# Kernel optimization log

Hardware: AMD Instinct MI355X
Metric: run time of the kernel (lower is better)

The kernel has to match this reference:

```python
import jax, jax.numpy as jnp
import numpy as np

C = 256
C8 = C // 8


def setup_inputs() -> dict:
    key = jax.random.key(0)
    ks = jax.random.split(key, 9)
    B, H, W = 4, 64, 64
    s = 1.0 / np.sqrt(C)
    return {
        "pre_feat": jax.random.normal(ks[0], (B, C, H, W), jnp.float32),
        "post_feat": jax.random.normal(ks[1], (B, C, H, W), jnp.float32),
        "Wq": jax.random.normal(ks[2], (C8, C), jnp.float32) * s,
        "bq": jnp.zeros((C8,), jnp.float32),
        "Wk": jax.random.normal(ks[3], (C8, C), jnp.float32) * s,
        "bk": jnp.zeros((C8,), jnp.float32),
        "Wv": jax.random.normal(ks[4], (C, C), jnp.float32) * s,
        "bv": jnp.zeros((C,), jnp.float32),
        "gamma": jnp.zeros((1,), jnp.float32),
    }


def reference(pre_feat, post_feat, Wq, bq, Wk, bk, Wv, bv, gamma):
    B, Cc, H, W = pre_feat.shape
    N = H * W
    pre = pre_feat.reshape(B, Cc, N)    # (B, C, N)
    post = post_feat.reshape(B, Cc, N)
    # 1x1 convs == per-pixel linear projections
    q = jnp.einsum('dc,bcn->bdn', Wq, post) + bq[None, :, None]  # (B, C8, N)
    k = jnp.einsum('dc,bcn->bdn', Wk, pre) + bk[None, :, None]   # (B, C8, N)
    v = jnp.einsum('dc,bcn->bdn', Wv, pre) + bv[None, :, None]   # (B, C, N)
    # energy[b,i,j] = <q[b,:,i], k[b,:,j]>  (unscaled)
    energy = jnp.einsum('bdi,bdj->bij', q, k)                    # (B, N, N)
    attention = jax.nn.softmax(energy, axis=-1)
    # out[b,c,i] = sum_j v[b,c,j] * attention[b,i,j]
    out = jnp.einsum('bcj,bij->bci', v, attention).reshape(B, Cc, H, W)
    return gamma[0] * out + post_feat
```

## Files before the change

kernel.cpp:

```cpp
#include <hip/hip_runtime.h>
#include <hip/hip_bf16.h>

#define Bn 4
#define Cn 256
#define Dn 32
#define Nn 4096

typedef __bf16 bf16x8 __attribute__((ext_vector_type(8)));
typedef float f32x4 __attribute__((ext_vector_type(4)));

__device__ __forceinline__ float bf2f(unsigned short u) {
  unsigned int v = ((unsigned int)u) << 16;
  return __builtin_bit_cast(float, v);
}
__device__ __forceinline__ unsigned short f2bf(float f) {
  unsigned int v = __builtin_bit_cast(unsigned int, f);
  v += 0x7FFFu + ((v >> 16) & 1u);
  return (unsigned short)(v >> 16);
}
__device__ __forceinline__ unsigned int pk2(float a, float b) {
  union { __hip_bfloat162 h; unsigned int u; } x;
  x.h = __float22bfloat162_rn(make_float2(a, b));
  return x.u;
}
__device__ __forceinline__ bf16x8 ldfrag(const unsigned short* p) {
  return __builtin_bit_cast(bf16x8, *(const uint4*)p);
}
__device__ __forceinline__ uint4 pack8(const float* p) {
  float4 a = *(const float4*)p;
  float4 b = *(const float4*)(p + 4);
  union { unsigned int u2[4]; uint4 u; } x;
  x.u2[0] = pk2(a.x, a.y); x.u2[1] = pk2(a.z, a.w);
  x.u2[2] = pk2(b.x, b.y); x.u2[3] = pk2(b.z, b.w);
  return x.u;
}
__device__ __forceinline__ bf16x8 ldfrag_f32(const float* p) {
  float4 a = *(const float4*)p;
  float4 b = *(const float4*)(p + 4);
  union { unsigned int u2[4]; bf16x8 v; } x;
  x.u2[0] = pk2(a.x, a.y); x.u2[1] = pk2(a.z, a.w);
  x.u2[2] = pk2(b.x, b.y); x.u2[3] = pk2(b.z, b.w);
  return x.v;
}
__device__ __forceinline__ void async16(unsigned short* lds, const unsigned short* g) {
  __builtin_amdgcn_global_load_lds(
      (const __attribute__((address_space(1))) unsigned int*)g,
      (__attribute__((address_space(3))) unsigned int*)lds, 16, 0, 0);
}

__global__ __launch_bounds__(256) void qkprep(
    const float* __restrict__ pre, const float* __restrict__ post,
    const float* __restrict__ Wq, const float* __restrict__ bq,
    const float* __restrict__ Wk, const float* __restrict__ bk,
    const float* __restrict__ Wv,
    unsigned short* __restrict__ Qt, unsigned short* __restrict__ Kt,
    unsigned short* __restrict__ preBf, unsigned short* __restrict__ WvBf)
{
  const int blk = blockIdx.x, tid = threadIdx.x;
  if (blk >= 512) {
    if (blk < 1024) {
      size_t base = ((size_t)(blk - 512) * 256 + tid) * 32;
#pragma unroll
      for (int u = 0; u < 4; u++)
        *(uint4*)(preBf + base + u * 8) = pack8(pre + base + u * 8);
    } else {
      size_t base = ((size_t)(blk - 1024) * 256 + tid) * 32;
#pragma unroll
      for (int u = 0; u < 4; u++)
        *(uint4*)(WvBf + base + u * 8) = pack8(Wv + base + u * 8);
    }
    return;
  }
  const int lane = tid & 63, w = tid >> 6;
  const int quad = lane >> 4, n16 = lane & 15;
  const int b = blk >> 7;
  const int i0 = (blk & 127) << 5;
  const int isub = w & 1, dh = w >> 1;
  const int i = i0 + isub * 16 + n16;

  const f32x4 zz = {0.f, 0.f, 0.f, 0.f};
  f32x4 aq = zz, ak = zz;
  const float* postB = post + (size_t)b * Cn * Nn + i;
  const float* preB  = pre  + (size_t)b * Cn * Nn + i;

#pragma unroll
  for (int kc = 0; kc < 8; kc++) {
    const int c0 = kc * 32 + quad * 8;
    const float* pp = postB + (size_t)c0 * Nn;
    const float* pr = preB + (size_t)c0 * Nn;
    union { unsigned int u2[4]; bf16x8 v; } bp, bq8;
#pragma unroll
    for (int e2 = 0; e2 < 4; e2++) {
      float p0 = pp[(size_t)(2 * e2) * Nn], p1 = pp[(size_t)(2 * e2 + 1) * Nn];
      float r0 = pr[(size_t)(2 * e2) * Nn], r1 = pr[(size_t)(2 * e2 + 1) * Nn];
      bp.u2[e2] = pk2(p0, p1);
      bq8.u2[e2] = pk2(r0, r1);
    }
    bf16x8 awq = ldfrag_f32(Wq + (size_t)(dh * 16 + n16) * Cn + kc * 32 + quad * 8);
    bf16x8 awk = ldfrag_f32(Wk + (size_t)(dh * 16 + n16) * Cn + kc * 32 + quad * 8);
    aq = __builtin_amdgcn_mfma_f32_16x16x32_bf16(awq, bp.v, aq, 0, 0, 0);
    ak = __builtin_amdgcn_mfma_f32_16x16x32_bf16(awk, bq8.v, ak, 0, 0, 0);
  }
  const float LOG2E = 1.44269504f;
  union { unsigned short s[4]; uint2 u; } oq, ok;
#pragma unroll
  for (int r = 0; r < 4; r++) {
    int d = dh * 16 + quad * 4 + r;
    oq.s[r] = f2bf((aq[r] + bq[d]) * LOG2E);
    ok.s[r] = f2bf(ak[r] + bk[d]);
  }
  *(uint2*)(Qt + ((size_t)b * Nn + i) * Dn + dh * 16 + quad * 4) = oq.u;
  *(uint2*)(Kt + ((size_t)b * Nn + i) * Dn + dh * 16 + quad * 4) = ok.u;
}

__global__ __launch_bounds__(256, 4) void flash_attn(
    const unsigned short* __restrict__ Qt, const unsigned short* __restrict__ Kt,
    const unsigned short* __restrict__ preBf,
    unsigned short* __restrict__ Opart, float* __restrict__ Lpart)
{
  __shared__ __align__(16) unsigned short sX[256 * 64];
  __shared__ __align__(16) unsigned short Pl[64 * 64];

  const int tid = threadIdx.x;
  const int lane = tid & 63, w = tid >> 6;
  const int quad = lane >> 4, n16 = lane & 15;
  const int b = blockIdx.x >> 8;
  const int js = (blockIdx.x >> 6) & 3;
  const int it = blockIdx.x & 63;
  const int i0 = it * 64;
  const int jbase = js * 1024;

  const bf16x8 qf = ldfrag(Qt + ((size_t)b * Nn + i0 + w * 16 + n16) * Dn + quad * 8);

  const f32x4 zz = {0.f, 0.f, 0.f, 0.f};
  f32x4 acc[4][4];
#pragma unroll
  for (int sub = 0; sub < 4; sub++)
#pragma unroll
    for (int ct = 0; ct < 4; ct++) acc[sub][ct] = zz;
  float lrow = 0.f;

  const size_t laneoff = (size_t)(lane >> 3) * Nn + (size_t)(((lane & 7) ^ (lane >> 3)) << 3);
  const unsigned short* preB = preBf + (size_t)b * Cn * Nn + laneoff;
  const int xsw = n16 & 7;
  const int xoff0 = (quad ^ xsw) << 3;
  const int xoff1 = ((4 + quad) ^ xsw) << 3;
  const int psw = (n16 & 7) << 3;

  for (int t = 0; t < 16; ++t) {
    const int j0 = jbase + t * 64;
    __syncthreads();
#pragma unroll
    for (int k = 0; k < 8; k++) {
      const int rb = (k * 4 + w) * 8;
      async16(sX + rb * 64 + (lane << 3), preB + (size_t)rb * Nn + j0);
    }
    {
      f32x4 sc[4];
#pragma unroll
      for (int jt = 0; jt < 4; jt++) {
        bf16x8 akf = ldfrag(Kt + ((size_t)b * Nn + j0 + jt * 16 + n16) * Dn + quad * 8);
        sc[jt] = __builtin_amdgcn_mfma_f32_16x16x32_bf16(akf, qf, zz, 0, 0, 0);
      }
      float ps = 0.f;
#pragma unroll
      for (int jt = 0; jt < 4; jt++) {
        float p0 = exp2f(fminf(sc[jt][0], 101.f));
        float p1 = exp2f(fminf(sc[jt][1], 101.f));
        float p2 = exp2f(fminf(sc[jt][2], 101.f));
        float p3 = exp2f(fminf(sc[jt][3], 101.f));
        ps += (p0 + p1) + (p2 + p3);
        union { unsigned int u2[2]; uint2 u; } pk;
        pk.u2[0] = pk2(p0, p1);
        pk.u2[1] = pk2(p2, p3);
        *(uint2*)&Pl[(size_t)(w * 16 + n16) * 64 + ((jt * 16 + quad * 4) ^ psw)] = pk.u;
      }
      ps += __shfl_xor(ps, 16);
      ps += __shfl_xor(ps, 32);
      lrow += ps;
    }
    __syncthreads();

#pragma unroll
    for (int kc = 0; kc < 2; kc++) {
      const int xo = kc ? xoff1 : xoff0;
      bf16x8 pB[4];
#pragma unroll
      for (int sub = 0; sub < 4; sub++)
        pB[sub] = ldfrag(&Pl[(size_t)(sub * 16 + n16) * 64 + ((kc * 32 + quad * 8) ^ psw)]);
#pragma unroll
      for (int ct = 0; ct < 4; ct++) {
        const int crow = w * 64 + ct * 16 + n16;
        bf16x8 av = ldfrag(&sX[crow * 64 + xo]);
        acc[0][ct] = __builtin_amdgcn_mfma_f32_16x16x32_bf16(av, pB[0], acc[0][ct], 0, 0, 0);
        acc[1][ct] = __builtin_amdgcn_mfma_f32_16x16x32_bf16(av, pB[1], acc[1][ct], 0, 0, 0);
        acc[2][ct] = __builtin_amdgcn_mfma_f32_16x16x32_bf16(av, pB[2], acc[2][ct], 0, 0, 0);
        acc[3][ct] = __builtin_amdgcn_mfma_f32_16x16x32_bf16(av, pB[3], acc[3][ct], 0, 0, 0);
      }
    }
  }

  const size_t pbase = (size_t)(js * 4 + b) * Nn;
  if (quad == 0) Lpart[pbase + i0 + w * 16 + n16] = lrow;
#pragma unroll
  for (int sub = 0; sub < 4; sub++) {
    const int i = i0 + sub * 16 + n16;
#pragma unroll
    for (int ct = 0; ct < 4; ct++) {
      union { unsigned int u2[2]; uint2 u; } pk;
      pk.u2[0] = pk2(acc[sub][ct][0], acc[sub][ct][1]);
      pk.u2[1] = pk2(acc[sub][ct][2], acc[sub][ct][3]);
      *(uint2*)(Opart + (pbase + i) * 256 + w * 64 + ct * 16 + quad * 4) = pk.u;
    }
  }
}

__global__ __launch_bounds__(256) void combine(
    const unsigned short* __restrict__ Opart, const float* __restrict__ Lpart,
    const unsigned short* __restrict__ WvBf, const float* __restrict__ bv,
    const float* __restrict__ post, const float* __restrict__ gamma,
    float* __restrict__ out)
{
  __shared__ __align__(16) unsigned short sU[16 * 264];
  __shared__ float sL[16];

  const int tid = threadIdx.x;
  const int lane = tid & 63, w = tid >> 6;
  const int quad = lane >> 4, n16 = lane & 15;
  const int b = blockIdx.x >> 8;
  const int i0 = (blockIdx.x & 255) << 4;

  if (tid < 16) {
    float l = 0.f;
#pragma unroll
    for (int js = 0; js < 4; js++) l += Lpart[(size_t)(js * 4 + b) * Nn + i0 + tid];
    sL[tid] = 1.f / l;
  }
  __syncthreads();

#pragma unroll
  for (int pass = 0; pass < 2; pass++) {
    const int s = tid + pass * 256;
    const int il = s >> 5, c8 = (s & 31) << 3;
    const float inv = sL[il];
    float a[8] = {0.f, 0.f, 0.f, 0.f, 0.f, 0.f, 0.f, 0.f};
#pragma unroll
    for (int js = 0; js < 4; js++) {
      uint4 uu = *(const uint4*)(Opart + ((size_t)(js * 4 + b) * Nn + i0 + il) * 256 + c8);
      const unsigned short* us = (const unsigned short*)&uu;
#pragma unroll
      for (int e = 0; e < 8; e++) a[e] += bf2f(us[e]);
    }
    union { unsigned int u2[4]; uint4 u; } pk;
#pragma unroll
    for (int e2 = 0; e2 < 4; e2++) pk.u2[e2] = pk2(a[2 * e2] * inv, a[2 * e2 + 1] * inv);
    *(uint4*)&sU[il * 264 + c8] = pk.u;
  }
  __syncthreads();

  bf16x8 ub[8];
#pragma unroll
  for (int kc = 0; kc < 8; kc++)
    ub[kc] = ldfrag(&sU[n16 * 264 + kc * 32 + quad * 8]);

  const float g = gamma[0];
  const f32x4 zz = {0.f, 0.f, 0.f, 0.f};
#pragma unroll
  for (int e = 0; e < 4; e++) {
    const int ct2 = w * 4 + e;
    f32x4 o = zz;
#pragma unroll
    for (int kc = 0; kc < 8; kc++) {
      bf16x8 awv = ldfrag(WvBf + (size_t)(ct2 * 16 + n16) * Cn + kc * 32 + quad * 8);
      o = __builtin_amdgcn_mfma_f32_16x16x32_bf16(awv, ub[kc], o, 0, 0, 0);
    }
#pragma unroll
    for (int r = 0; r < 4; r++) {
      const int c = ct2 * 16 + quad * 4 + r;
      const size_t addr = ((size_t)b * Cn + c) * Nn + i0 + n16;
      out[addr] = g * (o[r] + bv[c]) + post[addr];
    }
  }
}

extern "C" void kernel_launch(void* const* d_in, const int* in_sizes, int n_in,
                              void* d_out, int out_size, void* d_ws, size_t ws_size,
                              hipStream_t stream) {
  const float* pre   = (const float*)d_in[0];
  const float* post  = (const float*)d_in[1];
  const float* Wq    = (const float*)d_in[2];
  const float* bq    = (const float*)d_in[3];
  const float* Wk    = (const float*)d_in[4];
  const float* bk    = (const float*)d_in[5];
  const float* Wv    = (const float*)d_in[6];
  const float* bv    = (const float*)d_in[7];
  const float* gamma = (const float*)d_in[8];
  float* out = (float*)d_out;

  unsigned short* ws = (unsigned short*)d_ws;
  unsigned short* Qt    = ws;
  unsigned short* Kt    = Qt + (size_t)Bn * Nn * Dn;
  unsigned short* preBf = Kt + (size_t)Bn * Nn * Dn;
  unsigned short* WvBf  = preBf + (size_t)Bn * Cn * Nn;
  float* Lpart = (float*)(WvBf + Cn * Cn);
  unsigned short* Opart = (unsigned short*)(Lpart + 4 * Bn * Nn);

  qkprep<<<1032, 256, 0, stream>>>(pre, post, Wq, bq, Wk, bk, Wv,
                                   Qt, Kt, preBf, WvBf);
  flash_attn<<<1024, 256, 0, stream>>>(Qt, Kt, preBf, Opart, Lpart);
  combine<<<1024, 256, 0, stream>>>(Opart, Lpart, WvBf, bv, post, gamma, out);
}
```

Baseline: 188.2 us.

## Compute V projection before attention and simplify combine to transpose-add

```diff
diff --git a/kernel.cpp b/kernel.cpp
--- a/kernel.cpp
+++ b/kernel.cpp
@@ -25,14 +25,6 @@
 }
 __device__ __forceinline__ bf16x8 ldfrag(const unsigned short* p) {
   return __builtin_bit_cast(bf16x8, *(const uint4*)p);
-}
-__device__ __forceinline__ uint4 pack8(const float* p) {
-  float4 a = *(const float4*)p;
-  float4 b = *(const float4*)(p + 4);
-  union { unsigned int u2[4]; uint4 u; } x;
-  x.u2[0] = pk2(a.x, a.y); x.u2[1] = pk2(a.z, a.w);
-  x.u2[2] = pk2(b.x, b.y); x.u2[3] = pk2(b.z, b.w);
-  return x.u;
 }
 __device__ __forceinline__ bf16x8 ldfrag_f32(const float* p) {
   float4 a = *(const float4*)p;
@@ -52,33 +44,58 @@
     const float* __restrict__ pre, const float* __restrict__ post,
     const float* __restrict__ Wq, const float* __restrict__ bq,
     const float* __restrict__ Wk, const float* __restrict__ bk,
-    const float* __restrict__ Wv,
+    const float* __restrict__ Wv, const float* __restrict__ bv,
     unsigned short* __restrict__ Qt, unsigned short* __restrict__ Kt,
-    unsigned short* __restrict__ preBf, unsigned short* __restrict__ WvBf)
+    unsigned short* __restrict__ VBf)
 {
   const int blk = blockIdx.x, tid = threadIdx.x;
-  if (blk >= 512) {
-    if (blk < 1024) {
-      size_t base = ((size_t)(blk - 512) * 256 + tid) * 32;
-#pragma unroll
-      for (int u = 0; u < 4; u++)
-        *(uint4*)(preBf + base + u * 8) = pack8(pre + base + u * 8);
-    } else {
-      size_t base = ((size_t)(blk - 1024) * 256 + tid) * 32;
-#pragma unroll
-      for (int u = 0; u < 4; u++)
-        *(uint4*)(WvBf + base + u * 8) = pack8(Wv + base + u * 8);
-    }
-    return;
-  }
   const int lane = tid & 63, w = tid >> 6;
   const int quad = lane >> 4, n16 = lane & 15;
+  const f32x4 zz = {0.f, 0.f, 0.f, 0.f};
+
+  if (blk >= 512) {
+    const int vb = blk - 512;
+    const int b = vb >> 7;
+    const int j0 = (vb & 127) << 5;
+    const int jsub = w & 1, chalf = w >> 1;
+    const int j = j0 + jsub * 16 + n16;
+
+    f32x4 acc[8];
+#pragma unroll
+    for (int ct = 0; ct < 8; ct++) acc[ct] = zz;
+
+    const float* preB = pre + (size_t)b * Cn * Nn + j;
+#pragma unroll
+    for (int kc = 0; kc < 8; kc++) {
+      const float* pr = preB + (size_t)(kc * 32 + quad * 8) * Nn;
+      union { unsigned int u2[4]; bf16x8 v; } bp;
+#pragma unroll
+      for (int e2 = 0; e2 < 4; e2++) {
+        float r0 = pr[(size_t)(2 * e2) * Nn], r1 = pr[(size_t)(2 * e2 + 1) * Nn];
+        bp.u2[e2] = pk2(r0, r1);
+      }
+#pragma unroll
+      for (int ct = 0; ct < 8; ct++) {
+        bf16x8 aw = ldfrag_f32(Wv + (size_t)(chalf * 128 + ct * 16 + n16) * Cn + kc * 32 + quad * 8);
+        acc[ct] = __builtin_amdgcn_mfma_f32_16x16x32_bf16(aw, bp.v, acc[ct], 0, 0, 0);
+      }
+    }
+#pragma unroll
+    for (int ct = 0; ct < 8; ct++) {
+#pragma unroll
+      for (int r = 0; r < 4; r++) {
+        const int c = chalf * 128 + ct * 16 + quad * 4 + r;
+        VBf[((size_t)b * Cn + c) * Nn + j] = f2bf(acc[ct][r] + bv[c]);
+      }
+    }
+    return;
+  }
+
   const int b = blk >> 7;
   const int i0 = (blk & 127) << 5;
   const int isub = w & 1, dh = w >> 1;
   const int i = i0 + isub * 16 + n16;
 
-  const f32x4 zz = {0.f, 0.f, 0.f, 0.f};
   f32x4 aq = zz, ak = zz;
   const float* postB = post + (size_t)b * Cn * Nn + i;
   const float* preB  = pre  + (size_t)b * Cn * Nn + i;
@@ -115,7 +132,7 @@
 
 __global__ __launch_bounds__(256, 4) void flash_attn(
     const unsigned short* __restrict__ Qt, const unsigned short* __restrict__ Kt,
-    const unsigned short* __restrict__ preBf,
+    const unsigned short* __restrict__ VBf,
     unsigned short* __restrict__ Opart, float* __restrict__ Lpart)
 {
   __shared__ __align__(16) unsigned short sX[256 * 64];
@@ -141,7 +158,7 @@
   float lrow = 0.f;
 
   const size_t laneoff = (size_t)(lane >> 3) * Nn + (size_t)(((lane & 7) ^ (lane >> 3)) << 3);
-  const unsigned short* preB = preBf + (size_t)b * Cn * Nn + laneoff;
+  const unsigned short* preB = VBf + (size_t)b * Cn * Nn + laneoff;
   const int xsw = n16 & 7;
   const int xoff0 = (quad ^ xsw) << 3;
   const int xoff1 = ((4 + quad) ^ xsw) << 3;
@@ -217,20 +234,19 @@
 
 __global__ __launch_bounds__(256) void combine(
     const unsigned short* __restrict__ Opart, const float* __restrict__ Lpart,
-    const unsigned short* __restrict__ WvBf, const float* __restrict__ bv,
     const float* __restrict__ post, const float* __restrict__ gamma,
     float* __restrict__ out)
 {
-  __shared__ __align__(16) unsigned short sU[16 * 264];
-  __shared__ float sL[16];
+  __shared__ float sT[64 * 65];
+  __shared__ float sL[64];
 
   const int tid = threadIdx.x;
-  const int lane = tid & 63, w = tid >> 6;
-  const int quad = lane >> 4, n16 = lane & 15;
   const int b = blockIdx.x >> 8;
-  const int i0 = (blockIdx.x & 255) << 4;
-
-  if (tid < 16) {
+  const int rest = blockIdx.x & 255;
+  const int i0 = (rest >> 2) * 64;
+  const int c0 = (rest & 3) * 64;
+
+  if (tid < 64) {
     float l = 0.f;
 #pragma unroll
     for (int js = 0; js < 4; js++) l += Lpart[(size_t)(js * 4 + b) * Nn + i0 + tid];
@@ -240,46 +256,35 @@
 
 #pragma unroll
   for (int pass = 0; pass < 2; pass++) {
-    const int s = tid + pass * 256;
-    const int il = s >> 5, c8 = (s & 31) << 3;
+    const int il = (tid >> 3) + pass * 32;
+    const int c8 = (tid & 7) << 3;
+    float a[8] = {0.f, 0.f, 0.f, 0.f, 0.f, 0.f, 0.f, 0.f};
+#pragma unroll
+    for (int js = 0; js < 4; js++) {
+      uint4 uu = *(const uint4*)(Opart + ((size_t)(js * 4 + b) * Nn + i0 + il) * 256 + c0 + c8);
+      const unsigned short* us = (const unsigned short*)&uu;
+#pragma unroll
+      for (int e = 0; e < 8; e++) a[e] += bf2f(us[e]);
+    }
     const float inv = sL[il];
-    float a[8] = {0.f, 0.f, 0.f, 0.f, 0.f, 0.f, 0.f, 0.f};
-#pragma unroll
-    for (int js = 0; js < 4; js++) {
-      uint4 uu = *(const uint4*)(Opart + ((size_t)(js * 4 + b) * Nn + i0 + il) * 256 + c8);
-      const unsigned short* us = (const unsigned short*)&uu;
-#pragma unroll
-      for (int e = 0; e < 8; e++) a[e] += bf2f(us[e]);
-    }
-    union { unsigned int u2[4]; uint4 u; } pk;
-#pragma unroll
-    for (int e2 = 0; e2 < 4; e2++) pk.u2[e2] = pk2(a[2 * e2] * inv, a[2 * e2 + 1] * inv);
-    *(uint4*)&sU[il * 264 + c8] = pk.u;
+#pragma unroll
+    for (int e = 0; e < 8; e++) sT[(c8 + e) * 65 + il] = a[e] * inv;
   }
   __syncthreads();
 
-  bf16x8 ub[8];
-#pragma unroll
-  for (int kc = 0; kc < 8; kc++)
-    ub[kc] = ldfrag(&sU[n16 * 264 + kc * 32 + quad * 8]);
-
   const float g = gamma[0];
-  const f32x4 zz = {0.f, 0.f, 0.f, 0.f};
-#pragma unroll
-  for (int e = 0; e < 4; e++) {
-    const int ct2 = w * 4 + e;
-    f32x4 o = zz;
-#pragma unroll
-    for (int kc = 0; kc < 8; kc++) {
-      bf16x8 awv = ldfrag(WvBf + (size_t)(ct2 * 16 + n16) * Cn + kc * 32 + quad * 8);
-      o = __builtin_amdgcn_mfma_f32_16x16x32_bf16(awv, ub[kc], o, 0, 0, 0);
-    }
-#pragma unroll
-    for (int r = 0; r < 4; r++) {
-      const int c = ct2 * 16 + quad * 4 + r;
-      const size_t addr = ((size_t)b * Cn + c) * Nn + i0 + n16;
-      out[addr] = g * (o[r] + bv[c]) + post[addr];
-    }
+#pragma unroll
+  for (int itr = 0; itr < 4; itr++) {
+    const int slot = tid + itr * 256;
+    const int cr = slot >> 4, i4 = (slot & 15) << 2;
+    const size_t addr = ((size_t)b * Cn + c0 + cr) * Nn + i0 + i4;
+    float4 pp = *(const float4*)(post + addr);
+    float4 ov;
+    ov.x = g * sT[cr * 65 + i4 + 0] + pp.x;
+    ov.y = g * sT[cr * 65 + i4 + 1] + pp.y;
+    ov.z = g * sT[cr * 65 + i4 + 2] + pp.z;
+    ov.w = g * sT[cr * 65 + i4 + 3] + pp.w;
+    *(float4*)(out + addr) = ov;
   }
 }
 
@@ -300,13 +305,12 @@
   unsigned short* ws = (unsigned short*)d_ws;
   unsigned short* Qt    = ws;
   unsigned short* Kt    = Qt + (size_t)Bn * Nn * Dn;
-  unsigned short* preBf = Kt + (size_t)Bn * Nn * Dn;
-  unsigned short* WvBf  = preBf + (size_t)Bn * Cn * Nn;
-  float* Lpart = (float*)(WvBf + Cn * Cn);
+  unsigned short* VBf   = Kt + (size_t)Bn * Nn * Dn;
+  float* Lpart = (float*)(VBf + (size_t)Bn * Cn * Nn);
   unsigned short* Opart = (unsigned short*)(Lpart + 4 * Bn * Nn);
 
-  qkprep<<<1032, 256, 0, stream>>>(pre, post, Wq, bq, Wk, bk, Wv,
-                                   Qt, Kt, preBf, WvBf);
-  flash_attn<<<1024, 256, 0, stream>>>(Qt, Kt, preBf, Opart, Lpart);
-  combine<<<1024, 256, 0, stream>>>(Opart, Lpart, WvBf, bv, post, gamma, out);
-}
+  qkprep<<<1024, 256, 0, stream>>>(pre, post, Wq, bq, Wk, bk, Wv, bv,
+                                   Qt, Kt, VBf);
+  flash_attn<<<1024, 256, 0, stream>>>(Qt, Kt, VBf, Opart, Lpart);
+  combine<<<1024, 256, 0, stream>>>(Opart, Lpart, post, gamma, out);
+}
```

Result: slower. 209.2 us (+11.2%).
